# Performance work log

Measured on AMD Instinct MI355X. Metric: run time of the kernel, lower is better.

## Reference

```python
import jax, jax.numpy as jnp
import numpy as np

P = 2          # inverse-distance power (init arg p)
EPS = 1e-6     # clamp floor on dis**p
B, N, D, VDIM = 4096, 8192, 512, 512


def setup_inputs() -> dict:
    key = jax.random.key(0)
    kb, kk, kv = jax.random.split(key, 3)
    b = jax.random.normal(kb, (B, D), dtype=jnp.float32)
    K = jax.random.normal(kk, (N, D), dtype=jnp.float32)   # stacked sample keys
    V = jax.random.normal(kv, (N, VDIM), dtype=jnp.float32)  # stacked sample values
    return {"b": b, "K": K, "V": V}


def reference(b, K, V):
    # Pairwise Euclidean distances via the expansion ||b-k||^2 = ||b||^2 + ||k||^2 - 2 b.k
    # (avoids materializing the [B, N, D] difference tensor).
    b_sq = jnp.sum(b * b, axis=1, keepdims=True)          # [B, 1]
    k_sq = jnp.sum(K * K, axis=1)[None, :]                # [1, N]
    d2 = b_sq + k_sq - 2.0 * (b @ K.T)                    # [B, N]
    dist = jnp.sqrt(jnp.maximum(d2, 0.0))                 # torch.norm(k - b, dim=1)
    w = 1.0 / jnp.maximum(dist ** P, EPS)                 # 1 / clamp(dis^p, 1e-6)
    sum_w = jnp.sum(w, axis=1, keepdims=True)             # [B, 1]
    sum_v = w @ V                                         # sum_n w[b,n] * V[n,:]
    return sum_v / sum_w
```

## Files before the change

### kernel.cpp

```cpp
#include <hip/hip_runtime.h>
#include <stdint.h>

typedef __attribute__((ext_vector_type(2))) float  f32x2;
typedef __attribute__((ext_vector_type(4))) float  f32x4;
typedef __attribute__((ext_vector_type(2))) __bf16 bf16x2;
typedef __attribute__((ext_vector_type(8))) __bf16 bf16x8;

#define N_B    4096
#define N_K    8192
#define DDIM   512
#define VD     512
#define SPLITK 4

#define GLL(g, l) __builtin_amdgcn_global_load_lds(                      \
    (const __attribute__((address_space(1))) void*)(g),                  \
    (__attribute__((address_space(3))) void*)(l), 16, 0, 0)

__global__ void prep_rows(const float* __restrict__ src, __bf16* __restrict__ dst,
                          float* __restrict__ sq)
{
  const int row = blockIdx.x;
  const int tid = threadIdx.x;
  f32x2 v = ((const f32x2*)(src + (size_t)row * DDIM))[tid];
  float ss = v[0] * v[0] + v[1] * v[1];
  bf16x2 o; o[0] = (__bf16)v[0]; o[1] = (__bf16)v[1];
  ((bf16x2*)(dst + (size_t)row * DDIM))[tid] = o;
  #pragma unroll
  for (int m = 1; m < 64; m <<= 1) ss += __shfl_xor(ss, m);
  __shared__ float red[4];
  if ((tid & 63) == 0) red[tid >> 6] = ss;
  __syncthreads();
  if (tid == 0) sq[row] = red[0] + red[1] + red[2] + red[3];
}

__global__ void prep_vT(const float* __restrict__ V, __bf16* __restrict__ VT)
{
  __shared__ __bf16 t[64][72];
  const int n0 = blockIdx.x * 64;
  const int d0 = blockIdx.y * 64;
  const int tid = threadIdx.x;
  const int lr = tid >> 4, lc = tid & 15;
  #pragma unroll
  for (int p = 0; p < 4; p++) {
    const int r = p * 16 + lr;
    f32x4 v = *(const f32x4*)(V + (size_t)(n0 + r) * VD + d0 + lc * 4);
    t[r][lc * 4 + 0] = (__bf16)v[0];
    t[r][lc * 4 + 1] = (__bf16)v[1];
    t[r][lc * 4 + 2] = (__bf16)v[2];
    t[r][lc * 4 + 3] = (__bf16)v[3];
  }
  __syncthreads();
  const int od = tid >> 6, oc = tid & 63;
  #pragma unroll
  for (int p = 0; p < 16; p++) {
    const int d = p * 4 + od;
    VT[(size_t)(d0 + d) * N_K + n0 + oc] = t[oc][d];
  }
}

template<int MODE>
__global__ void __launch_bounds__(256, 2)
gemm_bt(const __bf16* __restrict__ Amat, const __bf16* __restrict__ Bmat,
        const int ldaE, const int ldbE, const int kPerSplit,
        const float* __restrict__ bsq, const float* __restrict__ ksq,
        __bf16* __restrict__ Wout, float* __restrict__ sumw,
        float* __restrict__ Pout)
{
  __shared__ __bf16 Asm[128 * 64];
  __shared__ __bf16 Bsm[128 * 64];

  const int tid  = threadIdx.x;
  const int wid  = tid >> 6;
  const int lane = tid & 63;
  const int wm = wid >> 1, wn = wid & 1;
  const int r15 = lane & 15, hi = lane >> 4;

  const int m0 = blockIdx.y * 128;
  const int n0 = blockIdx.x * 128;
  const long kBegin = (long)blockIdx.z * kPerSplit;

  const int srow   = lane >> 3;
  const int schunk = (lane & 7) ^ srow;

  const __bf16* aSrc = Amat + (size_t)(m0 + wid * 32 + srow) * ldaE + kBegin + schunk * 8;
  const __bf16* bSrc = Bmat + (size_t)(n0 + wid * 32 + srow) * ldbE + kBegin + schunk * 8;
  __bf16* aDst = &Asm[wid * 32 * 64];
  __bf16* bDst = &Bsm[wid * 32 * 64];

  const f32x4 fzero = {0.f, 0.f, 0.f, 0.f};
  f32x4 acc[4][4];
  #pragma unroll
  for (int i = 0; i < 4; i++)
    #pragma unroll
    for (int j = 0; j < 4; j++) acc[i][j] = fzero;

  for (int k0 = 0; k0 < kPerSplit; k0 += 64) {
    __syncthreads();
    #pragma unroll
    for (int i = 0; i < 4; i++) {
      GLL(aSrc + (size_t)i * 8 * ldaE + k0, aDst + i * 8 * 64);
      GLL(bSrc + (size_t)i * 8 * ldbE + k0, bDst + i * 8 * 64);
    }
    __syncthreads();
    #pragma unroll
    for (int kk = 0; kk < 2; kk++) {
      bf16x8 af[4], bfr[4];
      #pragma unroll
      for (int mf = 0; mf < 4; mf++) {
        const int cs = ((kk << 2) + hi) ^ (r15 & 7);
        af[mf] = *(const bf16x8*)((const char*)Asm +
                   (wm * 64 + mf * 16 + r15) * 128 + cs * 16);
      }
      #pragma unroll
      for (int nf = 0; nf < 4; nf++) {
        const int cs = ((kk << 2) + hi) ^ (r15 & 7);
        bfr[nf] = *(const bf16x8*)((const char*)Bsm +
                    (wn * 64 + nf * 16 + r15) * 128 + cs * 16);
      }
      #pragma unroll
      for (int mf = 0; mf < 4; mf++)
        #pragma unroll
        for (int nf = 0; nf < 4; nf++)
          acc[mf][nf] = __builtin_amdgcn_mfma_f32_16x16x32_bf16(
              af[mf], bfr[nf], acc[mf][nf], 0, 0, 0);
    }
  }

  if constexpr (MODE == 0) {
    float kq[4];
    #pragma unroll
    for (int nf = 0; nf < 4; nf++) kq[nf] = ksq[n0 + wn * 64 + nf * 16 + r15];
    #pragma unroll
    for (int mf = 0; mf < 4; mf++) {
      const int rowb = m0 + wm * 64 + mf * 16 + hi * 4;
      const f32x4 bq = *(const f32x4*)(bsq + rowb);
      float rsum[4] = {0.f, 0.f, 0.f, 0.f};
      #pragma unroll
      for (int nf = 0; nf < 4; nf++) {
        const int col = n0 + wn * 64 + nf * 16 + r15;
        #pragma unroll
        for (int r = 0; r < 4; r++) {
          const float d2 = bq[r] + kq[nf] - 2.0f * acc[mf][nf][r];
          const float w  = 1.0f / fmaxf(d2, 1e-6f);
          rsum[r] += w;
          Wout[(size_t)(rowb + r) * N_K + col] = (__bf16)w;
        }
      }
      #pragma unroll
      for (int r = 0; r < 4; r++) {
        float tsum = rsum[r];
        tsum += __shfl_xor(tsum, 1);
        tsum += __shfl_xor(tsum, 2);
        tsum += __shfl_xor(tsum, 4);
        tsum += __shfl_xor(tsum, 8);
        if (r15 == 0) atomicAdd(&sumw[rowb + r], tsum);
      }
    }
  } else {
    float* op = Pout + (size_t)blockIdx.z * N_B * VD;
    #pragma unroll
    for (int mf = 0; mf < 4; mf++) {
      const int rowb = m0 + wm * 64 + mf * 16 + hi * 4;
      #pragma unroll
      for (int nf = 0; nf < 4; nf++) {
        const int col = n0 + wn * 64 + nf * 16 + r15;
        #pragma unroll
        for (int r = 0; r < 4; r++)
          op[(size_t)(rowb + r) * VD + col] = acc[mf][nf][r];
      }
    }
  }
}

__global__ void reduce_norm(const float* __restrict__ part, const float* __restrict__ sumw,
                            float* __restrict__ out)
{
  const int idx = blockIdx.x * 256 + threadIdx.x;
  const size_t stride = (size_t)N_B * VD / 4;
  const f32x4* p = (const f32x4*)part;
  f32x4 s = p[idx] + p[idx + stride] + p[idx + 2 * stride] + p[idx + 3 * stride];
  const float inv = 1.0f / sumw[idx >> 7];
  ((f32x4*)out)[idx] = s * inv;
}

extern "C" void kernel_launch(void* const* d_in, const int* in_sizes, int n_in,
                              void* d_out, int out_size, void* d_ws, size_t ws_size,
                              hipStream_t stream)
{
  const float* b = (const float*)d_in[0];
  const float* K = (const float*)d_in[1];
  const float* V = (const float*)d_in[2];
  float* out = (float*)d_out;
  (void)in_sizes; (void)n_in; (void)out_size; (void)ws_size;

  char* ws = (char*)d_ws;
  size_t off = 0;
  auto alloc = [&](size_t bytes) -> void* {
    void* p = ws + off;
    off += (bytes + 255) & ~(size_t)255;
    return p;
  };
  __bf16* b_bf  = (__bf16*)alloc((size_t)N_B * DDIM * 2);
  __bf16* K_bf  = (__bf16*)alloc((size_t)N_K * DDIM * 2);
  __bf16* V_T   = (__bf16*)alloc((size_t)VD * N_K * 2);
  float*  b_sq  = (float*)alloc((size_t)N_B * 4);
  float*  k_sq  = (float*)alloc((size_t)N_K * 4);
  float*  sum_w = (float*)alloc((size_t)N_B * 4);
  __bf16* w_bf  = (__bf16*)alloc((size_t)N_B * N_K * 2);
  float*  part  = (float*)alloc((size_t)SPLITK * N_B * VD * 4);

  hipMemsetAsync(sum_w, 0, N_B * 4, stream);
  prep_rows<<<N_B, 256, 0, stream>>>(b, b_bf, b_sq);
  prep_rows<<<N_K, 256, 0, stream>>>(K, K_bf, k_sq);
  prep_vT<<<dim3(N_K / 64, VD / 64), 256, 0, stream>>>(V, V_T);
  gemm_bt<0><<<dim3(N_K / 128, N_B / 128, 1), 256, 0, stream>>>(
      b_bf, K_bf, DDIM, DDIM, DDIM, b_sq, k_sq, w_bf, sum_w, nullptr);
  gemm_bt<1><<<dim3(VD / 128, N_B / 128, SPLITK), 256, 0, stream>>>(
      w_bf, V_T, N_K, N_K, N_K / SPLITK, nullptr, nullptr, nullptr, nullptr, part);
  reduce_norm<<<(N_B * VD / 4) / 256, 256, 0, stream>>>(part, sum_w, out);
}
```

Measured before the change: 213.2 us.

## Double-buffer LDS tiles and replace split-K partials with atomic accumulation

The bf16 GEMM kernel now uses two LDS buffers per operand, so global-to-LDS loads for the next K tile are issued before the MFMAs on the current tile, with one barrier per iteration instead of two. The second GEMM's split-K factor goes from 4 to 8. Its partial results are atomically added straight into the zeroed output instead of a partials buffer, and a lighter normalize kernel replaces the sum-and-normalize reduction. This removes the large partial-buffer write and read. In exchange it adds millions of fp32 global atomics, doubles LDS per block, and makes the summation order nondeterministic.

```diff
diff --git a/kernel.cpp b/kernel.cpp
--- a/kernel.cpp
+++ b/kernel.cpp
@@ -10,7 +10,7 @@
 #define N_K    8192
 #define DDIM   512
 #define VD     512
-#define SPLITK 4
+#define SPLITK 8
 
 #define GLL(g, l) __builtin_amdgcn_global_load_lds(                      \
     (const __attribute__((address_space(1))) void*)(g),                  \
@@ -66,8 +66,8 @@
         __bf16* __restrict__ Wout, float* __restrict__ sumw,
         float* __restrict__ Pout)
 {
-  __shared__ __bf16 Asm[128 * 64];
-  __shared__ __bf16 Bsm[128 * 64];
+  __shared__ __bf16 Asm[2][128 * 64];
+  __shared__ __bf16 Bsm[2][128 * 64];
 
   const int tid  = threadIdx.x;
   const int wid  = tid >> 6;
@@ -84,8 +84,15 @@
 
   const __bf16* aSrc = Amat + (size_t)(m0 + wid * 32 + srow) * ldaE + kBegin + schunk * 8;
   const __bf16* bSrc = Bmat + (size_t)(n0 + wid * 32 + srow) * ldbE + kBegin + schunk * 8;
-  __bf16* aDst = &Asm[wid * 32 * 64];
-  __bf16* bDst = &Bsm[wid * 32 * 64];
+  const int dstOff = wid * 32 * 64;
+
+  auto stage = [&](int buf, int k0) {
+    #pragma unroll
+    for (int i = 0; i < 4; i++) {
+      GLL(aSrc + (size_t)i * 8 * ldaE + k0, &Asm[buf][dstOff + i * 8 * 64]);
+      GLL(bSrc + (size_t)i * 8 * ldbE + k0, &Bsm[buf][dstOff + i * 8 * 64]);
+    }
+  };
 
   const f32x4 fzero = {0.f, 0.f, 0.f, 0.f};
   f32x4 acc[4][4];
@@ -94,27 +101,25 @@
     #pragma unroll
     for (int j = 0; j < 4; j++) acc[i][j] = fzero;
 
-  for (int k0 = 0; k0 < kPerSplit; k0 += 64) {
-    __syncthreads();
-    #pragma unroll
-    for (int i = 0; i < 4; i++) {
-      GLL(aSrc + (size_t)i * 8 * ldaE + k0, aDst + i * 8 * 64);
-      GLL(bSrc + (size_t)i * 8 * ldbE + k0, bDst + i * 8 * 64);
-    }
-    __syncthreads();
+  const int nt = kPerSplit / 64;
+  stage(0, 0);
+  __syncthreads();
+  int cur = 0;
+  for (int t = 0; t < nt; t++) {
+    if (t + 1 < nt) stage(cur ^ 1, (t + 1) * 64);
     #pragma unroll
     for (int kk = 0; kk < 2; kk++) {
       bf16x8 af[4], bfr[4];
       #pragma unroll
       for (int mf = 0; mf < 4; mf++) {
         const int cs = ((kk << 2) + hi) ^ (r15 & 7);
-        af[mf] = *(const bf16x8*)((const char*)Asm +
+        af[mf] = *(const bf16x8*)((const char*)&Asm[cur][0] +
                    (wm * 64 + mf * 16 + r15) * 128 + cs * 16);
       }
       #pragma unroll
       for (int nf = 0; nf < 4; nf++) {
         const int cs = ((kk << 2) + hi) ^ (r15 & 7);
-        bfr[nf] = *(const bf16x8*)((const char*)Bsm +
+        bfr[nf] = *(const bf16x8*)((const char*)&Bsm[cur][0] +
                     (wn * 64 + nf * 16 + r15) * 128 + cs * 16);
       }
       #pragma unroll
@@ -124,6 +129,8 @@
           acc[mf][nf] = __builtin_amdgcn_mfma_f32_16x16x32_bf16(
               af[mf], bfr[nf], acc[mf][nf], 0, 0, 0);
     }
+    __syncthreads();
+    cur ^= 1;
   }
 
   if constexpr (MODE == 0) {
@@ -157,7 +164,6 @@
       }
     }
   } else {
-    float* op = Pout + (size_t)blockIdx.z * N_B * VD;
     #pragma unroll
     for (int mf = 0; mf < 4; mf++) {
       const int rowb = m0 + wm * 64 + mf * 16 + hi * 4;
@@ -166,21 +172,18 @@
         const int col = n0 + wn * 64 + nf * 16 + r15;
         #pragma unroll
         for (int r = 0; r < 4; r++)
-          op[(size_t)(rowb + r) * VD + col] = acc[mf][nf][r];
-      }
-    }
-  }
-}
-
-__global__ void reduce_norm(const float* __restrict__ part, const float* __restrict__ sumw,
-                            float* __restrict__ out)
+          atomicAdd(&Pout[(size_t)(rowb + r) * VD + col], acc[mf][nf][r]);
+      }
+    }
+  }
+}
+
+__global__ void normalize(float* __restrict__ out, const float* __restrict__ sumw)
 {
   const int idx = blockIdx.x * 256 + threadIdx.x;
-  const size_t stride = (size_t)N_B * VD / 4;
-  const f32x4* p = (const f32x4*)part;
-  f32x4 s = p[idx] + p[idx + stride] + p[idx + 2 * stride] + p[idx + 3 * stride];
+  f32x4 v = ((f32x4*)out)[idx];
   const float inv = 1.0f / sumw[idx >> 7];
-  ((f32x4*)out)[idx] = s * inv;
+  ((f32x4*)out)[idx] = v * inv;
 }
 
 extern "C" void kernel_launch(void* const* d_in, const int* in_sizes, int n_in,
@@ -191,7 +194,7 @@
   const float* K = (const float*)d_in[1];
   const float* V = (const float*)d_in[2];
   float* out = (float*)d_out;
-  (void)in_sizes; (void)n_in; (void)out_size; (void)ws_size;
+  (void)in_sizes; (void)n_in; (void)ws_size;
 
   char* ws = (char*)d_ws;
   size_t off = 0;
@@ -207,15 +210,15 @@
   float*  k_sq  = (float*)alloc((size_t)N_K * 4);
   float*  sum_w = (float*)alloc((size_t)N_B * 4);
   __bf16* w_bf  = (__bf16*)alloc((size_t)N_B * N_K * 2);
-  float*  part  = (float*)alloc((size_t)SPLITK * N_B * VD * 4);
 
   hipMemsetAsync(sum_w, 0, N_B * 4, stream);
+  hipMemsetAsync(out, 0, (size_t)out_size * 4, stream);
   prep_rows<<<N_B, 256, 0, stream>>>(b, b_bf, b_sq);
   prep_rows<<<N_K, 256, 0, stream>>>(K, K_bf, k_sq);
   prep_vT<<<dim3(N_K / 64, VD / 64), 256, 0, stream>>>(V, V_T);
   gemm_bt<0><<<dim3(N_K / 128, N_B / 128, 1), 256, 0, stream>>>(
       b_bf, K_bf, DDIM, DDIM, DDIM, b_sq, k_sq, w_bf, sum_w, nullptr);
   gemm_bt<1><<<dim3(VD / 128, N_B / 128, SPLITK), 256, 0, stream>>>(
-      w_bf, V_T, N_K, N_K, N_K / SPLITK, nullptr, nullptr, nullptr, nullptr, part);
-  reduce_norm<<<(N_B * VD / 4) / 256, 256, 0, stream>>>(part, sum_w, out);
-}
+      w_bf, V_T, N_K, N_K, N_K / SPLITK, nullptr, nullptr, nullptr, nullptr, out);
+  normalize<<<(N_B * VD / 4) / 256, 256, 0, stream>>>(out, sum_w);
+}
```

Result: slower. 277.5 us (+30.2%).
